# Kernel optimization log

Measured on AMD Instinct MI355X. Metric: run time of the kernel, lower is better.

The kernel has to match this reference:

```python
import jax, jax.numpy as jnp
import numpy as np

N_WIRES = 4
N_LAYERS = 2
BSZ = 4096


def _gate(p):
    # combined single-qubit gate RX(p2) @ RZ(p1) @ RY(p0)  (RY applied first)
    a, b, c = p[0] * 0.5, p[1] * 0.5, p[2] * 0.5
    ca, sa = jnp.cos(a), jnp.sin(a)
    ry = jnp.stack([jnp.stack([ca, -sa]), jnp.stack([sa, ca])]).astype(jnp.complex64)
    eb = (jnp.cos(b) - 1j * jnp.sin(b)).astype(jnp.complex64)  # e^{-i b}
    zero = jnp.zeros((), jnp.complex64)
    rz = jnp.stack([jnp.stack([eb, zero]), jnp.stack([zero, jnp.conj(eb)])])
    cc, sc = jnp.cos(c), jnp.sin(c)
    rx = jnp.stack([jnp.stack([cc + 0j, -1j * sc]), jnp.stack([-1j * sc, cc + 0j])]).astype(jnp.complex64)
    return rx @ rz @ ry


def _apply1(state, U, w):
    # state: (N,2,2,2,2); apply 2x2 gate U on wire w
    s = jnp.moveaxis(state, w + 1, 4)
    s = jnp.einsum('nijka,ba->nijkb', s, U)
    return jnp.moveaxis(s, 4, w + 1)


def _cnot(state, c, t):
    s = jnp.moveaxis(state, (c + 1, t + 1), (1, 2))
    s = jnp.stack([s[:, 0], jnp.flip(s[:, 1], axis=1)], axis=1)
    return jnp.moveaxis(s, (1, 2), (c + 1, t + 1))


def _quanv(x, params):
    bsz = x.shape[0]
    # extract 2x2 patches in the same order as the torch loop:
    # [x[r,c], x[r,c+1], x[r+1,c], x[r+1,c+1]], row-major over (r,c)
    p = x.reshape(bsz, 14, 2, 14, 2).transpose(0, 1, 3, 2, 4).reshape(bsz * 196, 4)
    h = p * 0.5
    v = jnp.stack([jnp.cos(h), jnp.sin(h)], axis=-1).astype(jnp.complex64)  # (N,4,2): RY(patch)|0>
    state = jnp.einsum('na,nb,nc,nd->nabcd', v[:, 0], v[:, 1], v[:, 2], v[:, 3])
    for l in range(N_LAYERS):
        for w in range(N_WIRES):
            state = _apply1(state, _gate(params[l, w]), w)
        for w in range(N_WIRES - 1):
            state = _cnot(state, w, w + 1)
        state = _cnot(state, N_WIRES - 1, 0)
    probs = state.real ** 2 + state.imag ** 2  # (N,2,2,2,2)
    z = jnp.array([1.0, -1.0], jnp.float32)
    exps = []
    for w in range(N_WIRES):
        axes = tuple(i for i in range(1, 5) if i != w + 1)
        exps.append(probs.sum(axes) @ z)  # <Z_w>, shape (N,)
    # (N,4) -> (bsz, 196, 4) -> (bsz, 784), patch-major / wire-minor like torch.cat
    return jnp.stack(exps, axis=-1).reshape(bsz, 196 * N_WIRES)


def setup_inputs() -> dict:
    key = jax.random.key(0)
    k1, k2 = jax.random.split(key)
    x = jax.random.uniform(k1, (BSZ, 28, 28), dtype=jnp.float32)
    params = jax.random.normal(k2, (N_LAYERS, N_WIRES, 3), dtype=jnp.float32)
    return {"x": x, "params": params}


def reference(x, params):
    return _quanv(x, params)
```

## Files before the change

kernel.cpp:

```cpp
#include <hip/hip_runtime.h>


__device__ __forceinline__ float2 cmul(float2 a, float2 b) {
    return make_float2(fmaf(a.x, b.x, -(a.y * b.y)),
                       fmaf(a.x, b.y,   a.y * b.x));
}
__device__ __forceinline__ float2 cfma(float2 a, float2 b, float2 c) {
    return make_float2(fmaf(a.x, b.x, fmaf(-a.y, b.y, c.x)),
                       fmaf(a.x, b.y, fmaf( a.y, b.x, c.y)));
}

__global__ __launch_bounds__(256) void quanv_kernel(
        const float* __restrict__ x,
        const float* __restrict__ params,
        float* __restrict__ out)
{
    __shared__ float2 G[8][4];
    const int t = threadIdx.x;
    if (t < 8) {
        const float* p = params + t * 3;
        float sa, ca, sb, cb, sc, cc;
        __sincosf(0.5f * p[0], &sa, &ca);
        __sincosf(0.5f * p[1], &sb, &cb);
        __sincosf(0.5f * p[2], &sc, &cc);
        G[t][0] = make_float2( cc*ca*cb + sc*sa*sb, -cc*ca*sb - sc*sa*cb);
        G[t][1] = make_float2(-cc*sa*cb + sc*ca*sb,  cc*sa*sb - sc*ca*cb);
        G[t][2] = make_float2( cc*sa*cb - sc*ca*sb,  cc*sa*sb - sc*ca*cb);
        G[t][3] = make_float2( sa*sc*sb + cc*ca*cb,  sa*sc*cb + cc*ca*sb);
    }
    __syncthreads();

    const int gid = blockIdx.x * 256 + t;
    const int n = gid / 196;
    const int p = gid - n * 196;
    const int r = p / 14;
    const int c = p - r * 14;

    const float* xb = x + n * 784 + r * 56 + c * 2;
    const float2 top = *(const float2*)(xb);
    const float2 bot = *(const float2*)(xb + 28);

    float vc[4], vs[4];
    __sincosf(0.5f * top.x, &vs[0], &vc[0]);
    __sincosf(0.5f * top.y, &vs[1], &vc[1]);
    __sincosf(0.5f * bot.x, &vs[2], &vc[2]);
    __sincosf(0.5f * bot.y, &vs[3], &vc[3]);

    float2 s[16];
#pragma unroll
    for (int a = 0; a < 2; ++a)
#pragma unroll
        for (int b = 0; b < 2; ++b)
#pragma unroll
            for (int cc2 = 0; cc2 < 2; ++cc2)
#pragma unroll
                for (int d = 0; d < 2; ++d) {
                    float va = a ? vs[0] : vc[0];
                    float vb = b ? vs[1] : vc[1];
                    float vcx = cc2 ? vs[2] : vc[2];
                    float vd = d ? vs[3] : vc[3];
                    s[a * 8 + b * 4 + cc2 * 2 + d] = make_float2(va * vb * vcx * vd, 0.0f);
                }

#pragma unroll
    for (int l = 0; l < 2; ++l) {
#pragma unroll
        for (int w = 0; w < 4; ++w) {
            const int g = l * 4 + w;
            const float2 U00 = G[g][0], U01 = G[g][1], U10 = G[g][2], U11 = G[g][3];
            const int bit = 8 >> w;
#pragma unroll
            for (int i = 0; i < 16; ++i) {
                if (i & bit) continue;
                const float2 x0 = s[i], x1 = s[i | bit];
                s[i]       = cfma(U01, x1, cmul(U00, x0));
                s[i | bit] = cfma(U11, x1, cmul(U10, x0));
            }
        }
#pragma unroll
        for (int k = 0; k < 4; ++k) {
            const int bc = 8 >> k;
            const int bt = 8 >> ((k + 1) & 3);
#pragma unroll
            for (int i = 0; i < 16; ++i) {
                if ((i & bc) && !(i & bt)) {
                    const float2 tmp = s[i];
                    s[i] = s[i | bt];
                    s[i | bt] = tmp;
                }
            }
        }
    }

    float e0 = 0.f, e1 = 0.f, e2 = 0.f, e3 = 0.f;
#pragma unroll
    for (int i = 0; i < 16; ++i) {
        const float pr = fmaf(s[i].x, s[i].x, s[i].y * s[i].y);
        e0 += (i & 8) ? -pr : pr;
        e1 += (i & 4) ? -pr : pr;
        e2 += (i & 2) ? -pr : pr;
        e3 += (i & 1) ? -pr : pr;
    }

    *(float4*)(out + gid * 4) = make_float4(e0, e1, e2, e3);
}

extern "C" void kernel_launch(void* const* d_in, const int* in_sizes, int n_in,
                              void* d_out, int out_size, void* d_ws, size_t ws_size,
                              hipStream_t stream) {
    const float* x      = (const float*)d_in[0];
    const float* params = (const float*)d_in[1];
    float* out = (float*)d_out;

    const int npatch = 4096 * 196;
    quanv_kernel<<<npatch / 256, 256, 0, stream>>>(x, params, out);
}
```

Measured before the change: 81.79 us.

## Fold first gate layer into product-state init and factor expectation sums

Applies the first layer's single-qubit gates directly to each wire's RY-encoded 2-vector before forming the tensor product, so the initial state is built from pairwise complex products instead of running sixteen-amplitude gate updates for layer one. The expectation reduction is rewritten as shared partial sums over groups of probabilities. The sincos calls are split into separate sin/cos intrinsics. This cuts ALU work per patch, and the new accumulation order may change floating-point rounding slightly.

```diff
diff --git a/kernel.cpp b/kernel.cpp
--- a/kernel.cpp
+++ b/kernel.cpp
@@ -19,10 +19,10 @@
     const int t = threadIdx.x;
     if (t < 8) {
         const float* p = params + t * 3;
-        float sa, ca, sb, cb, sc, cc;
-        __sincosf(0.5f * p[0], &sa, &ca);
-        __sincosf(0.5f * p[1], &sb, &cb);
-        __sincosf(0.5f * p[2], &sc, &cc);
+        const float a = 0.5f * p[0], b = 0.5f * p[1], c = 0.5f * p[2];
+        const float sa = __sinf(a), ca = __cosf(a);
+        const float sb = __sinf(b), cb = __cosf(b);
+        const float sc = __sinf(c), cc = __cosf(c);
         G[t][0] = make_float2( cc*ca*cb + sc*sa*sb, -cc*ca*sb - sc*sa*cb);
         G[t][1] = make_float2(-cc*sa*cb + sc*ca*sb,  cc*sa*sb - sc*ca*cb);
         G[t][2] = make_float2( cc*sa*cb - sc*ca*sb,  cc*sa*sb - sc*ca*cb);
@@ -40,67 +40,86 @@
     const float2 top = *(const float2*)(xb);
     const float2 bot = *(const float2*)(xb + 28);
 
-    float vc[4], vs[4];
-    __sincosf(0.5f * top.x, &vs[0], &vc[0]);
-    __sincosf(0.5f * top.y, &vs[1], &vc[1]);
-    __sincosf(0.5f * bot.x, &vs[2], &vc[2]);
-    __sincosf(0.5f * bot.y, &vs[3], &vc[3]);
+    float pv[4] = {0.5f * top.x, 0.5f * top.y, 0.5f * bot.x, 0.5f * bot.y};
+    float2 wv[4][2];
+#pragma unroll
+    for (int w = 0; w < 4; ++w) {
+        const float cw = __cosf(pv[w]);
+        const float sw = __sinf(pv[w]);
+        const float2 U00 = G[w][0], U01 = G[w][1], U10 = G[w][2], U11 = G[w][3];
+        wv[w][0] = make_float2(fmaf(U01.x, sw, U00.x * cw), fmaf(U01.y, sw, U00.y * cw));
+        wv[w][1] = make_float2(fmaf(U11.x, sw, U10.x * cw), fmaf(U11.y, sw, U10.y * cw));
+    }
 
+    float2 ab[4], cd[4];
+#pragma unroll
+    for (int i = 0; i < 2; ++i)
+#pragma unroll
+        for (int j = 0; j < 2; ++j) {
+            ab[i * 2 + j] = cmul(wv[0][i], wv[1][j]);
+            cd[i * 2 + j] = cmul(wv[2][i], wv[3][j]);
+        }
     float2 s[16];
 #pragma unroll
-    for (int a = 0; a < 2; ++a)
+    for (int hi = 0; hi < 4; ++hi)
 #pragma unroll
-        for (int b = 0; b < 2; ++b)
-#pragma unroll
-            for (int cc2 = 0; cc2 < 2; ++cc2)
-#pragma unroll
-                for (int d = 0; d < 2; ++d) {
-                    float va = a ? vs[0] : vc[0];
-                    float vb = b ? vs[1] : vc[1];
-                    float vcx = cc2 ? vs[2] : vc[2];
-                    float vd = d ? vs[3] : vc[3];
-                    s[a * 8 + b * 4 + cc2 * 2 + d] = make_float2(va * vb * vcx * vd, 0.0f);
-                }
+        for (int lo = 0; lo < 4; ++lo)
+            s[hi * 4 + lo] = cmul(ab[hi], cd[lo]);
 
 #pragma unroll
-    for (int l = 0; l < 2; ++l) {
+    for (int k = 0; k < 4; ++k) {
+        const int bc = 8 >> k;
+        const int bt = 8 >> ((k + 1) & 3);
 #pragma unroll
-        for (int w = 0; w < 4; ++w) {
-            const int g = l * 4 + w;
-            const float2 U00 = G[g][0], U01 = G[g][1], U10 = G[g][2], U11 = G[g][3];
-            const int bit = 8 >> w;
+        for (int i = 0; i < 16; ++i)
+            if ((i & bc) && !(i & bt)) {
+                const float2 tmp = s[i]; s[i] = s[i | bt]; s[i | bt] = tmp;
+            }
+    }
+
 #pragma unroll
-            for (int i = 0; i < 16; ++i) {
-                if (i & bit) continue;
-                const float2 x0 = s[i], x1 = s[i | bit];
-                s[i]       = cfma(U01, x1, cmul(U00, x0));
-                s[i | bit] = cfma(U11, x1, cmul(U10, x0));
-            }
-        }
+    for (int w = 0; w < 4; ++w) {
+        const int g = 4 + w;
+        const float2 U00 = G[g][0], U01 = G[g][1], U10 = G[g][2], U11 = G[g][3];
+        const int bit = 8 >> w;
 #pragma unroll
-        for (int k = 0; k < 4; ++k) {
-            const int bc = 8 >> k;
-            const int bt = 8 >> ((k + 1) & 3);
-#pragma unroll
-            for (int i = 0; i < 16; ++i) {
-                if ((i & bc) && !(i & bt)) {
-                    const float2 tmp = s[i];
-                    s[i] = s[i | bt];
-                    s[i | bt] = tmp;
-                }
-            }
+        for (int i = 0; i < 16; ++i) {
+            if (i & bit) continue;
+            const float2 x0 = s[i], x1 = s[i | bit];
+            s[i]       = cfma(U01, x1, cmul(U00, x0));
+            s[i | bit] = cfma(U11, x1, cmul(U10, x0));
         }
     }
 
-    float e0 = 0.f, e1 = 0.f, e2 = 0.f, e3 = 0.f;
 #pragma unroll
-    for (int i = 0; i < 16; ++i) {
-        const float pr = fmaf(s[i].x, s[i].x, s[i].y * s[i].y);
-        e0 += (i & 8) ? -pr : pr;
-        e1 += (i & 4) ? -pr : pr;
-        e2 += (i & 2) ? -pr : pr;
-        e3 += (i & 1) ? -pr : pr;
+    for (int k = 0; k < 4; ++k) {
+        const int bc = 8 >> k;
+        const int bt = 8 >> ((k + 1) & 3);
+#pragma unroll
+        for (int i = 0; i < 16; ++i)
+            if ((i & bc) && !(i & bt)) {
+                const float2 tmp = s[i]; s[i] = s[i | bt]; s[i | bt] = tmp;
+            }
     }
+
+    float pr[16];
+#pragma unroll
+    for (int i = 0; i < 16; ++i)
+        pr[i] = fmaf(s[i].x, s[i].x, s[i].y * s[i].y);
+
+    const float t00 = pr[0] + pr[1] + pr[2]  + pr[3];
+    const float t01 = pr[4] + pr[5] + pr[6]  + pr[7];
+    const float t10 = pr[8] + pr[9] + pr[10] + pr[11];
+    const float t11 = pr[12] + pr[13] + pr[14] + pr[15];
+    const float e0 = (t00 + t01) - (t10 + t11);
+    const float e1 = (t00 - t01) + (t10 - t11);
+
+    const float u00 = pr[0] + pr[4] + pr[8]  + pr[12];
+    const float u01 = pr[1] + pr[5] + pr[9]  + pr[13];
+    const float u10 = pr[2] + pr[6] + pr[10] + pr[14];
+    const float u11 = pr[3] + pr[7] + pr[11] + pr[15];
+    const float e2 = (u00 + u01) - (u10 + u11);
+    const float e3 = (u00 - u01) + (u10 - u11);
 
     *(float4*)(out + gid * 4) = make_float4(e0, e1, e2, e3);
 }
```

Result: faster. 74.89 us (-8.4%).
